# Performance work log

Measured on AMD Instinct MI355X. Metric: run time of the kernel, lower is better.

Reference implementation:

```python
import jax, jax.numpy as jnp
import numpy as np

B, S, D, H = 2, 2048, 1024, 16
HD = D // H  # head_dim = 64
SCALE = HD ** -0.5


def setup_inputs() -> dict:
    key = jax.random.key(0)
    ks = jax.random.split(key, 5)
    s = 0.02
    return {
        "query": jax.random.normal(ks[0], (B, S, D), dtype=jnp.float32),
        "Wq": jax.random.normal(ks[1], (D, D), dtype=jnp.float32) * s,
        "bq": jnp.zeros((D,), dtype=jnp.float32),
        "Wk": jax.random.normal(ks[2], (D, D), dtype=jnp.float32) * s,
        "bk": jnp.zeros((D,), dtype=jnp.float32),
        "Wv": jax.random.normal(ks[3], (D, D), dtype=jnp.float32) * s,
        "bv": jnp.zeros((D,), dtype=jnp.float32),
        "Wo": jax.random.normal(ks[4], (D, D), dtype=jnp.float32) * s,
        "bo": jnp.zeros((D,), dtype=jnp.float32),
    }


def reference(query, Wq, bq, Wk, bk, Wv, bv, Wo, bo):
    b, s, _ = query.shape
    # QKV projections (self-attention: key = value = query)
    Q = (query @ Wq + bq).reshape(b, s, H, HD).transpose(0, 2, 1, 3)  # bhqd
    K = (query @ Wk + bk).reshape(b, s, H, HD).transpose(0, 2, 1, 3)  # bhkd
    V = (query @ Wv + bv).reshape(b, s, H, HD).transpose(0, 2, 1, 3)  # bhvd
    scores = jnp.einsum('bhqd,bhkd->bhqk', Q, K) * SCALE
    weights = jax.nn.softmax(scores, axis=-1)
    out = jnp.einsum('bhqk,bhkd->bhqd', weights, V)
    out = out.transpose(0, 2, 1, 3).reshape(b, s, D)
    return out @ Wo + bo
```

## Files before the change

### kernel.cpp

```cpp
#include <hip/hip_runtime.h>
#include <hip/hip_bf16.h>
#include <math.h>

#define B_ 2
#define S_ 2048
#define D_ 1024
#define H_ 16
#define HD_ 64
#define M_ (B_*S_)
#define C1_ 0.1803368798f

typedef float f32x4 __attribute__((ext_vector_type(4)));
typedef float f32x16 __attribute__((ext_vector_type(16)));
typedef short s16x8 __attribute__((ext_vector_type(8)));

__device__ __forceinline__ short f2bf(float f) {
  union { float f; unsigned u; } x; x.f = f;
  unsigned r = x.u + 0x7fffu + ((x.u >> 16) & 1u);
  return (short)(r >> 16);
}
__device__ __forceinline__ float bf2f(short v) {
  union { unsigned u; float f; } x; x.u = ((unsigned)(unsigned short)v) << 16;
  return x.f;
}
__device__ __forceinline__ unsigned cvt_pk_bf16(float a, float b) {
  unsigned r;
  asm("v_cvt_pk_bf16_f32 %0, %1, %2" : "=v"(r) : "v"(a), "v"(b));
  return r;
}
__device__ __forceinline__ float exp2_fast(float x) {
#if __has_builtin(__builtin_amdgcn_exp2f)
  return __builtin_amdgcn_exp2f(x);
#else
  float r; asm("v_exp_f32 %0, %1" : "=v"(r) : "v"(x)); return r;
#endif
}
__device__ __forceinline__ void gload_lds16(const void* g, void* l) {
  __builtin_amdgcn_global_load_lds(
      (const __attribute__((address_space(1))) void*)g,
      (__attribute__((address_space(3))) void*)l, 16, 0, 0);
}

__global__ __launch_bounds__(256) void k_prep(
    const float* __restrict__ query, short* __restrict__ xbf,
    const float* __restrict__ W0, const float* __restrict__ W1,
    const float* __restrict__ W2, const float* __restrict__ W3,
    short* __restrict__ T0, short* __restrict__ T1,
    short* __restrict__ T2, short* __restrict__ T3) {
  __shared__ short lt[64][72];
  const int blk = blockIdx.x;
  const int t = threadIdx.x;
  if (blk < 1024) {
    const int z = blk >> 8, tile = blk & 255;
    const float* W = z == 0 ? W0 : z == 1 ? W1 : z == 2 ? W2 : W3;
    short* Wt      = z == 0 ? T0 : z == 1 ? T1 : z == 2 ? T2 : T3;
    const int r0 = (tile >> 4) * 64;
    const int c0 = (tile & 15) * 64;
    const int rr = t >> 4, c4 = (t & 15) * 4;
    #pragma unroll
    for (int p = 0; p < 4; ++p) {
      int row = p * 16 + rr;
      f32x4 v = *reinterpret_cast<const f32x4*>(W + (size_t)(r0 + row) * D_ + c0 + c4);
      #pragma unroll
      for (int j = 0; j < 4; ++j) lt[c4 + j][row] = f2bf(v[j]);
    }
    __syncthreads();
    #pragma unroll
    for (int p = 0; p < 2; ++p) {
      int slot = p * 256 + t;
      int row = slot >> 3, s = slot & 7;
      s16x8 v = *reinterpret_cast<const s16x8*>(&lt[row][s * 8]);
      *reinterpret_cast<s16x8*>(Wt + (size_t)(c0 + row) * D_ + r0 + s * 8) = v;
    }
  } else {
    int i = ((blk - 1024) * 256 + t) * 8;
    f32x4 a = *reinterpret_cast<const f32x4*>(query + i);
    f32x4 b = *reinterpret_cast<const f32x4*>(query + i + 4);
    s16x8 v;
    v[0]=f2bf(a[0]); v[1]=f2bf(a[1]); v[2]=f2bf(a[2]); v[3]=f2bf(a[3]);
    v[4]=f2bf(b[0]); v[5]=f2bf(b[1]); v[6]=f2bf(b[2]); v[7]=f2bf(b[3]);
    *reinterpret_cast<s16x8*>(xbf + i) = v;
  }
}

__global__ __launch_bounds__(256) void k_gemm_qkv(
    const short* __restrict__ A,
    const short* __restrict__ WtQ, const short* __restrict__ WtK, const short* __restrict__ WtV,
    const float* __restrict__ bQ, const float* __restrict__ bK, const float* __restrict__ bV,
    short* __restrict__ Qo, short* __restrict__ Ko, short* __restrict__ Vto) {
  __shared__ __align__(16) char lds[32768];
  char* lA = lds;
  char* lB = lds + 16384;
  const int z = blockIdx.z;
  const short* Bt   = z == 0 ? WtQ : z == 1 ? WtK : WtV;
  const float* bias = z == 0 ? bQ  : z == 1 ? bK  : bV;
  const int t = threadIdx.x;
  const int lane = t & 63, wid = t >> 6;
  const int l15 = lane & 15, l4 = lane >> 4;
  const int wm = wid >> 1, wn = wid & 1;
  const int m0 = blockIdx.x * 128, n0 = blockIdx.y * 128;

  f32x4 acc[4][4];
  #pragma unroll
  for (int i = 0; i < 4; ++i)
    #pragma unroll
    for (int j = 0; j < 4; ++j) acc[i][j] = (f32x4){0.f, 0.f, 0.f, 0.f};

  for (int k0 = 0; k0 < D_; k0 += 64) {
    #pragma unroll
    for (int i = 0; i < 4; ++i) {
      int slot = t + i * 256;
      int row = slot >> 3, sw = (t & 7) ^ (row & 7);
      gload_lds16(A  + (size_t)(m0 + row) * D_ + k0 + sw * 8, lA + (i * 256 + wid * 64) * 16);
      gload_lds16(Bt + (size_t)(n0 + row) * D_ + k0 + sw * 8, lB + (i * 256 + wid * 64) * 16);
    }
    __syncthreads();
    #pragma unroll
    for (int ks = 0; ks < 2; ++ks) {
      s16x8 af[4], bf[4];
      #pragma unroll
      for (int mt = 0; mt < 4; ++mt) {
        int row = wm * 64 + mt * 16 + l15;
        af[mt] = *reinterpret_cast<const s16x8*>(lA + row * 128 + (((ks*4 + l4) ^ (row & 7)) * 16));
      }
      #pragma unroll
      for (int nt = 0; nt < 4; ++nt) {
        int row = wn * 64 + nt * 16 + l15;
        bf[nt] = *reinterpret_cast<const s16x8*>(lB + row * 128 + (((ks*4 + l4) ^ (row & 7)) * 16));
      }
      #pragma unroll
      for (int mt = 0; mt < 4; ++mt)
        #pragma unroll
        for (int nt = 0; nt < 4; ++nt)
          acc[mt][nt] = __builtin_amdgcn_mfma_f32_16x16x32_bf16(af[mt], bf[nt], acc[mt][nt], 0, 0, 0);
    }
    __syncthreads();
  }

  const float scale = (z == 0) ? C1_ : 1.f;
  #pragma unroll
  for (int nt = 0; nt < 4; ++nt) {
    int cl = wn * 64 + nt * 16 + l15;
    float bv = bias[n0 + cl];
    #pragma unroll
    for (int mt = 0; mt < 4; ++mt) {
      #pragma unroll
      for (int r = 0; r < 4; ++r) {
        int rl = wm * 64 + mt * 16 + l4 * 4 + r;
        short hv = f2bf((acc[mt][nt][r] + bv) * scale);
        if (z == 2) *reinterpret_cast<short*>(lds + cl * 256 + rl * 2) = hv;
        else        *reinterpret_cast<short*>(lds + rl * 256 + cl * 2) = hv;
      }
    }
  }
  __syncthreads();
  short* outp = (z == 0) ? Qo : (z == 1) ? Ko : Vto;
  const size_t ld   = (z == 2) ? (size_t)M_ : (size_t)D_;
  const int rowbase = (z == 2) ? n0 : m0;
  const int colbase = (z == 2) ? m0 : n0;
  #pragma unroll
  for (int p = 0; p < 8; ++p) {
    int slot = p * 256 + t;
    int row = slot >> 4, s = slot & 15;
    s16x8 v = *reinterpret_cast<const s16x8*>(lds + row * 256 + s * 16);
    *reinterpret_cast<s16x8*>(outp + (size_t)(rowbase + row) * ld + colbase + s * 8) = v;
  }
}

__global__ __launch_bounds__(256) void k_gemm_out(const short* __restrict__ A,
                                                  const short* __restrict__ Bt,
                                                  const float* __restrict__ bias,
                                                  float* __restrict__ C) {
  __shared__ __align__(16) char lA[128 * 128];
  __shared__ __align__(16) char lB[64 * 128];
  const int t = threadIdx.x;
  const int lane = t & 63, wid = t >> 6;
  const int l15 = lane & 15, l4 = lane >> 4;
  const int wm = wid >> 1, wn = wid & 1;
  const int m0 = blockIdx.x * 128, n0 = blockIdx.y * 64;

  f32x4 acc[4][2];
  #pragma unroll
  for (int i = 0; i < 4; ++i)
    #pragma unroll
    for (int j = 0; j < 2; ++j) acc[i][j] = (f32x4){0.f, 0.f, 0.f, 0.f};

  for (int k0 = 0; k0 < D_; k0 += 64) {
    #pragma unroll
    for (int i = 0; i < 4; ++i) {
      int slot = t + i * 256;
      int row = slot >> 3, sw = (t & 7) ^ (row & 7);
      gload_lds16(A + (size_t)(m0 + row) * D_ + k0 + sw * 8, lA + (i * 256 + wid * 64) * 16);
    }
    #pragma unroll
    for (int i = 0; i < 2; ++i) {
      int slot = t + i * 256;
      int row = slot >> 3, sw = (t & 7) ^ (row & 7);
      gload_lds16(Bt + (size_t)(n0 + row) * D_ + k0 + sw * 8, lB + (i * 256 + wid * 64) * 16);
    }
    __syncthreads();
    #pragma unroll
    for (int ks = 0; ks < 2; ++ks) {
      s16x8 af[4], bf[2];
      #pragma unroll
      for (int mt = 0; mt < 4; ++mt) {
        int row = wm * 64 + mt * 16 + l15;
        af[mt] = *reinterpret_cast<const s16x8*>(lA + row * 128 + (((ks*4 + l4) ^ (row & 7)) * 16));
      }
      #pragma unroll
      for (int nt = 0; nt < 2; ++nt) {
        int row = wn * 32 + nt * 16 + l15;
        bf[nt] = *reinterpret_cast<const s16x8*>(lB + row * 128 + (((ks*4 + l4) ^ (row & 7)) * 16));
      }
      #pragma unroll
      for (int mt = 0; mt < 4; ++mt)
        #pragma unroll
        for (int nt = 0; nt < 2; ++nt)
          acc[mt][nt] = __builtin_amdgcn_mfma_f32_16x16x32_bf16(af[mt], bf[nt], acc[mt][nt], 0, 0, 0);
    }
    __syncthreads();
  }
  #pragma unroll
  for (int nt = 0; nt < 2; ++nt) {
    int col = n0 + wn * 32 + nt * 16 + l15;
    float bv = bias[col];
    #pragma unroll
    for (int mt = 0; mt < 4; ++mt) {
      int row0 = m0 + wm * 64 + mt * 16 + l4 * 4;
      #pragma unroll
      for (int r = 0; r < 4; ++r)
        C[(size_t)(row0 + r) * D_ + col] = acc[mt][nt][r] + bv;
    }
  }
}

__global__ __launch_bounds__(256, 4) void k_attn(const short* __restrict__ Q,
                                                 const short* __restrict__ K,
                                                 const short* __restrict__ Vt,
                                                 short* __restrict__ U0,
                                                 short* __restrict__ U1,
                                                 float* __restrict__ lsum) {
  __shared__ __align__(16) char lds[32768];
  const int t = threadIdx.x;
  const int lane = t & 63, wid = t >> 6;
  const int l31 = lane & 31, hi = lane >> 5;
  const int orig = blockIdx.x;
  const int xcd = orig & 7, idx = orig >> 3;
  const int bh = xcd * 4 + (idx >> 5);
  const int rem = idx & 31;
  const int qblk = rem >> 1;
  const int half = rem & 1;
  const int b = bh >> 4, h = bh & 15;
  const int q0 = qblk * 128;
  const size_t qkbase = (size_t)b * S_ * D_ + h * HD_;
  const short* gK = K + qkbase + (size_t)(half * (S_ / 2)) * D_;
  const short* gVt = Vt + (size_t)(h * HD_) * M_ + (size_t)b * S_ + half * (S_ / 2);
  short* Up = half ? U1 : U0;

  s16x8 qf[4];
  {
    const short* qp = Q + qkbase + (size_t)(q0 + wid * 32 + l31) * D_ + hi * 8;
    qf[0] = *reinterpret_cast<const s16x8*>(qp);
    qf[1] = *reinterpret_cast<const s16x8*>(qp + 16);
    qf[2] = *reinterpret_cast<const s16x8*>(qp + 32);
    qf[3] = *reinterpret_cast<const s16x8*>(qp + 48);
  }

  f32x16 oa[2];
  #pragma unroll
  for (int i = 0; i < 16; ++i) { oa[0][i] = 0.f; oa[1][i] = 0.f; }
  float l_run = 0.f;

  const int tr3 = t >> 3;
  const int ssw8 = ((t & 7) ^ (tr3 & 7)) * 8;
  const size_t kSrc = (size_t)tr3 * D_ + ssw8;
  const size_t vSrc = (size_t)tr3 * M_ + ssw8;

  const int s7 = l31 & 7;
  const int rbase = l31 * 128;
  int soff[4];
  #pragma unroll
  for (int ks = 0; ks < 4; ++ks) soff[ks] = ((2 * ks + hi) ^ s7) * 16;

  auto stage = [&](int tl, int bb) {
    if (tl >= S_ / 128) return;
    const short* pk = gK + (size_t)(tl * 64) * D_ + kSrc;
    const short* pv = gVt + tl * 64 + vSrc;
    char* dK = lds + bb * 8192 + wid * 1024;
    char* dV = dK + 16384;
    gload_lds16(pk, dK);
    gload_lds16(pk + (size_t)32 * D_, dK + 4096);
    gload_lds16(pv, dV);
    gload_lds16(pv + (size_t)32 * M_, dV + 4096);
  };

  auto tileFn = [&](int bb, int tl) {
    stage(tl + 1, bb ^ 1);
    const char* bK = lds + bb * 8192;
    const char* bV = bK + 16384;

    f32x16 sc[2];
    #pragma unroll
    for (int i = 0; i < 16; ++i) { sc[0][i] = 0.f; sc[1][i] = 0.f; }
    __builtin_amdgcn_s_setprio(1);
    #pragma unroll
    for (int ks = 0; ks < 4; ++ks)
      #pragma unroll
      for (int blk = 0; blk < 2; ++blk) {
        s16x8 kf = *reinterpret_cast<const s16x8*>(bK + blk * 4096 + rbase + soff[ks]);
        sc[blk] = __builtin_amdgcn_mfma_f32_32x32x16_bf16(kf, qf[ks], sc[blk], 0, 0, 0);
      }
    __builtin_amdgcn_s_setprio(0);

    float rs = 0.f;
    unsigned pkA[2][4], pkB[2][4];
    #pragma unroll
    for (int blk = 0; blk < 2; ++blk)
      #pragma unroll
      for (int g = 0; g < 4; ++g) {
        float p0 = exp2_fast(sc[blk][4*g+0]), p1 = exp2_fast(sc[blk][4*g+1]);
        float p2 = exp2_fast(sc[blk][4*g+2]), p3 = exp2_fast(sc[blk][4*g+3]);
        rs += (p0 + p1) + (p2 + p3);
        pkA[blk][g] = cvt_pk_bf16(p0, p1);
        pkB[blk][g] = cvt_pk_bf16(p2, p3);
      }
    rs += __shfl_xor(rs, 32);
    l_run += rs;

    __builtin_amdgcn_s_setprio(1);
    #pragma unroll
    for (int sp = 0; sp < 4; ++sp) {
      const int blk = sp >> 1, su = sp & 1;
      unsigned a0 = pkA[blk][2*su],     a1 = pkB[blk][2*su];
      unsigned b0 = pkA[blk][2*su + 1], b1 = pkB[blk][2*su + 1];
      asm("v_permlane32_swap_b32 %0, %1" : "+v"(a0), "+v"(b0));
      asm("v_permlane32_swap_b32 %0, %1" : "+v"(a1), "+v"(b1));
      union { unsigned u[4]; s16x8 v; } pw;
      pw.u[0] = a0; pw.u[1] = a1; pw.u[2] = b0; pw.u[3] = b1;
      #pragma unroll
      for (int dblk = 0; dblk < 2; ++dblk) {
        s16x8 vf = *reinterpret_cast<const s16x8*>(bV + dblk * 4096 + rbase + soff[sp]);
        oa[dblk] = __builtin_amdgcn_mfma_f32_32x32x16_bf16(pw.v, vf, oa[dblk], 0, 0, 0);
      }
    }
    __builtin_amdgcn_s_setprio(0);
    __syncthreads();
  };

  stage(0, 0);
  __syncthreads();
  #pragma unroll 1
  for (int it = 0; it < S_ / 256; ++it) {
    tileFn(0, 2 * it);
    tileFn(1, 2 * it + 1);
  }

  char* myl = lds + wid * 4096;
  #pragma unroll
  for (int reg = 0; reg < 16; ++reg) {
    int qrow = (reg & 3) + 8 * (reg >> 2) + 4 * hi;
    *reinterpret_cast<short*>(myl + qrow * 128 + l31 * 2)        = f2bf(oa[0][reg]);
    *reinterpret_cast<short*>(myl + qrow * 128 + (32 + l31) * 2) = f2bf(oa[1][reg]);
  }
  #pragma unroll
  for (int i = 0; i < 4; ++i) {
    int slot = i * 64 + lane;
    int row = slot >> 3, s = slot & 7;
    s16x8 v = *reinterpret_cast<const s16x8*>(myl + slot * 16);
    *reinterpret_cast<s16x8*>(
        Up + qkbase + (size_t)(q0 + wid * 32 + row) * D_ + s * 8) = v;
  }
  if (hi == 0)
    lsum[((half * 32 + bh) << 11) + q0 + wid * 32 + l31] = l_run;
}

__global__ __launch_bounds__(256) void k_merge(const short* U0, const short* U1,
                                               const float* lsum, short* out) {
  int i = (blockIdx.x * 256 + threadIdx.x) * 8;
  int row = i >> 10;
  int col = i & 1023;
  int b = row >> 11, s = row & 2047;
  int bh = b * 16 + (col >> 6);
  float l0 = lsum[(bh << 11) + s];
  float l1 = lsum[((32 + bh) << 11) + s];
  float inv = 1.f / (l0 + l1);
  s16x8 u0 = *reinterpret_cast<const s16x8*>(U0 + i);
  s16x8 u1 = *reinterpret_cast<const s16x8*>(U1 + i);
  s16x8 r;
  #pragma unroll
  for (int j = 0; j < 8; ++j) r[j] = f2bf((bf2f(u0[j]) + bf2f(u1[j])) * inv);
  *reinterpret_cast<s16x8*>(out + i) = r;
}

extern "C" void kernel_launch(void* const* d_in, const int* in_sizes, int n_in,
                              void* d_out, int out_size, void* d_ws, size_t ws_size,
                              hipStream_t stream) {
  const float* query = (const float*)d_in[0];
  const float* Wq = (const float*)d_in[1];
  const float* bq = (const float*)d_in[2];
  const float* Wk = (const float*)d_in[3];
  const float* bk = (const float*)d_in[4];
  const float* Wv = (const float*)d_in[5];
  const float* bv = (const float*)d_in[6];
  const float* Wo = (const float*)d_in[7];
  const float* bo = (const float*)d_in[8];
  float* out = (float*)d_out;

  const size_t NE = (size_t)M_ * D_;
  short* ws   = (short*)d_ws;
  short* xbf  = ws;
  short* qbf  = ws + NE;
  short* kbf  = ws + 2 * NE;
  short* vtbf = ws + 3 * NE;
  short* aout = ws + 4 * NE;
  short* wtq  = ws + 5 * NE;
  short* wtk  = wtq + (size_t)D_ * D_;
  short* wtv  = wtk + (size_t)D_ * D_;
  short* wto  = wtv + (size_t)D_ * D_;

  short* U0 = aout;
  short* U1 = xbf;
  float* lsb = (float*)wtq;

  k_prep<<<3072, 256, 0, stream>>>(query, xbf, Wq, Wk, Wv, Wo, wtq, wtk, wtv, wto);

  k_gemm_qkv<<<dim3(M_ / 128, D_ / 128, 3), 256, 0, stream>>>(
      xbf, wtq, wtk, wtv, bq, bk, bv, qbf, kbf, vtbf);

  k_attn<<<1024, 256, 0, stream>>>(qbf, kbf, vtbf, U0, U1, lsb);
  k_merge<<<(int)(NE / (8 * 256)), 256, 0, stream>>>(U0, U1, lsb, aout);

  k_gemm_out<<<dim3(M_ / 128, D_ / 64), 256, 0, stream>>>(aout, wto, bo, out);
}
```

Measured before the change: 118.0 us.

## Double-buffer LDS tiles in QKV and output projection GEMMs

```diff
diff --git a/kernel.cpp b/kernel.cpp
--- a/kernel.cpp
+++ b/kernel.cpp
@@ -88,9 +88,7 @@
     const short* __restrict__ WtQ, const short* __restrict__ WtK, const short* __restrict__ WtV,
     const float* __restrict__ bQ, const float* __restrict__ bK, const float* __restrict__ bV,
     short* __restrict__ Qo, short* __restrict__ Ko, short* __restrict__ Vto) {
-  __shared__ __align__(16) char lds[32768];
-  char* lA = lds;
-  char* lB = lds + 16384;
+  __shared__ __align__(16) char lds[65536];
   const int z = blockIdx.z;
   const short* Bt   = z == 0 ? WtQ : z == 1 ? WtK : WtV;
   const float* bias = z == 0 ? bQ  : z == 1 ? bK  : bV;
@@ -106,27 +104,37 @@
     #pragma unroll
     for (int j = 0; j < 4; ++j) acc[i][j] = (f32x4){0.f, 0.f, 0.f, 0.f};
 
-  for (int k0 = 0; k0 < D_; k0 += 64) {
+  auto stage = [&](int k0, int buf) {
+    char* base = lds + buf * 32768;
     #pragma unroll
     for (int i = 0; i < 4; ++i) {
       int slot = t + i * 256;
       int row = slot >> 3, sw = (t & 7) ^ (row & 7);
-      gload_lds16(A  + (size_t)(m0 + row) * D_ + k0 + sw * 8, lA + (i * 256 + wid * 64) * 16);
-      gload_lds16(Bt + (size_t)(n0 + row) * D_ + k0 + sw * 8, lB + (i * 256 + wid * 64) * 16);
-    }
-    __syncthreads();
+      gload_lds16(A  + (size_t)(m0 + row) * D_ + k0 + sw * 8, base + (i * 256 + wid * 64) * 16);
+      gload_lds16(Bt + (size_t)(n0 + row) * D_ + k0 + sw * 8, base + 16384 + (i * 256 + wid * 64) * 16);
+    }
+  };
+
+  stage(0, 0);
+  __syncthreads();
+
+  int buf = 0;
+  for (int k0 = 0; k0 < D_; k0 += 64, buf ^= 1) {
+    if (k0 + 64 < D_) stage(k0 + 64, buf ^ 1);
+    const char* bA = lds + buf * 32768;
+    const char* bB = bA + 16384;
     #pragma unroll
     for (int ks = 0; ks < 2; ++ks) {
       s16x8 af[4], bf[4];
       #pragma unroll
       for (int mt = 0; mt < 4; ++mt) {
         int row = wm * 64 + mt * 16 + l15;
-        af[mt] = *reinterpret_cast<const s16x8*>(lA + row * 128 + (((ks*4 + l4) ^ (row & 7)) * 16));
+        af[mt] = *reinterpret_cast<const s16x8*>(bA + row * 128 + (((ks*4 + l4) ^ (row & 7)) * 16));
       }
       #pragma unroll
       for (int nt = 0; nt < 4; ++nt) {
         int row = wn * 64 + nt * 16 + l15;
-        bf[nt] = *reinterpret_cast<const s16x8*>(lB + row * 128 + (((ks*4 + l4) ^ (row & 7)) * 16));
+        bf[nt] = *reinterpret_cast<const s16x8*>(bB + row * 128 + (((ks*4 + l4) ^ (row & 7)) * 16));
       }
       #pragma unroll
       for (int mt = 0; mt < 4; ++mt)
@@ -171,8 +179,7 @@
                                                   const short* __restrict__ Bt,
                                                   const float* __restrict__ bias,
                                                   float* __restrict__ C) {
-  __shared__ __align__(16) char lA[128 * 128];
-  __shared__ __align__(16) char lB[64 * 128];
+  __shared__ __align__(16) char lds[49152];
   const int t = threadIdx.x;
   const int lane = t & 63, wid = t >> 6;
   const int l15 = lane & 15, l4 = lane >> 4;
@@ -185,32 +192,43 @@
     #pragma unroll
     for (int j = 0; j < 2; ++j) acc[i][j] = (f32x4){0.f, 0.f, 0.f, 0.f};
 
-  for (int k0 = 0; k0 < D_; k0 += 64) {
+  auto stage = [&](int k0, int buf) {
+    char* base = lds + buf * 24576;
     #pragma unroll
     for (int i = 0; i < 4; ++i) {
       int slot = t + i * 256;
       int row = slot >> 3, sw = (t & 7) ^ (row & 7);
-      gload_lds16(A + (size_t)(m0 + row) * D_ + k0 + sw * 8, lA + (i * 256 + wid * 64) * 16);
+      gload_lds16(A + (size_t)(m0 + row) * D_ + k0 + sw * 8, base + (i * 256 + wid * 64) * 16);
     }
     #pragma unroll
     for (int i = 0; i < 2; ++i) {
       int slot = t + i * 256;
       int row = slot >> 3, sw = (t & 7) ^ (row & 7);
-      gload_lds16(Bt + (size_t)(n0 + row) * D_ + k0 + sw * 8, lB + (i * 256 + wid * 64) * 16);
-    }
-    __syncthreads();
+      gload_lds16(Bt + (size_t)(n0 + row) * D_ + k0 + sw * 8,
+                  base + 16384 + (i * 256 + wid * 64) * 16);
+    }
+  };
+
+  stage(0, 0);
+  __syncthreads();
+
+  int buf = 0;
+  for (int k0 = 0; k0 < D_; k0 += 64, buf ^= 1) {
+    if (k0 + 64 < D_) stage(k0 + 64, buf ^ 1);
+    const char* bA = lds + buf * 24576;
+    const char* bB = bA + 16384;
     #pragma unroll
     for (int ks = 0; ks < 2; ++ks) {
       s16x8 af[4], bf[2];
       #pragma unroll
       for (int mt = 0; mt < 4; ++mt) {
         int row = wm * 64 + mt * 16 + l15;
-        af[mt] = *reinterpret_cast<const s16x8*>(lA + row * 128 + (((ks*4 + l4) ^ (row & 7)) * 16));
+        af[mt] = *reinterpret_cast<const s16x8*>(bA + row * 128 + (((ks*4 + l4) ^ (row & 7)) * 16));
       }
       #pragma unroll
       for (int nt = 0; nt < 2; ++nt) {
         int row = wn * 32 + nt * 16 + l15;
-        bf[nt] = *reinterpret_cast<const s16x8*>(lB + row * 128 + (((ks*4 + l4) ^ (row & 7)) * 16));
+        bf[nt] = *reinterpret_cast<const s16x8*>(bB + row * 128 + (((ks*4 + l4) ^ (row & 7)) * 16));
       }
       #pragma unroll
       for (int mt = 0; mt < 4; ++mt)
```

Result: faster. 102.2 us (-13.4%).
